# Kernel tuning notes

Measured on AMD Instinct MI355X. Metric: run time of the kernel, lower is better.

Reference implementation:

```python
import jax, jax.numpy as jnp
from jax import lax
import numpy as np

D_MODEL = 512
D_STATE = 16
D_CONV = 4
EXPAND = 2
D_INNER = EXPAND * D_MODEL  # 1024
DT_RANK = (D_MODEL + 15) // 16  # 32
FF_DIM = 1024
N_LAYERS = 2
B, L = 2, 2048


def setup_inputs() -> dict:
    key = jax.random.key(0)
    ks = jax.random.split(key, 16)
    s = 0.02
    x = jax.random.normal(ks[0], (B, L, D_MODEL), jnp.float32)
    in_proj_w = jax.random.normal(ks[1], (N_LAYERS, 2 * D_INNER, D_MODEL), jnp.float32) * s
    conv_w = jax.random.normal(ks[2], (N_LAYERS, D_INNER, D_CONV), jnp.float32) * 0.3
    conv_b = jax.random.normal(ks[3], (N_LAYERS, D_INNER), jnp.float32) * s
    x_proj_w = jax.random.normal(ks[4], (N_LAYERS, DT_RANK + 2 * D_STATE, D_INNER), jnp.float32) * s
    dt_proj_w = jax.random.normal(ks[5], (N_LAYERS, D_INNER, DT_RANK), jnp.float32) * s
    dt_proj_b = jax.random.normal(ks[6], (N_LAYERS, D_INNER), jnp.float32) * 0.5 - 4.0
    A_log = jnp.log(jnp.broadcast_to(jnp.arange(1, D_STATE + 1, dtype=jnp.float32), (N_LAYERS, D_INNER, D_STATE)))
    Dp = jnp.ones((N_LAYERS, D_INNER), jnp.float32)
    out_proj_w = jax.random.normal(ks[7], (N_LAYERS, D_MODEL, D_INNER), jnp.float32) * s
    mlp_w1 = jax.random.normal(ks[8], (FF_DIM, D_MODEL), jnp.float32) * s
    mlp_b1 = jnp.zeros((FF_DIM,), jnp.float32)
    mlp_w2 = jax.random.normal(ks[9], (D_MODEL, FF_DIM), jnp.float32) * s
    mlp_b2 = jnp.zeros((D_MODEL,), jnp.float32)
    return dict(x=x, in_proj_w=in_proj_w, conv_w=conv_w, conv_b=conv_b,
                x_proj_w=x_proj_w, dt_proj_w=dt_proj_w, dt_proj_b=dt_proj_b,
                A_log=A_log, Dp=Dp, out_proj_w=out_proj_w,
                mlp_w1=mlp_w1, mlp_b1=mlp_b1, mlp_w2=mlp_w2, mlp_b2=mlp_b2)


def _mamba_layer(x, ipw, cw, cb, xpw, dpw, dpb, Al, Dv, opw):
    # x: [B, L, d_model]
    b, l, _ = x.shape
    xz = jnp.einsum('bld,ed->ble', x, ipw)           # [B, L, 2*d_inner]
    xin, z = jnp.split(xz, 2, axis=-1)
    # causal depthwise conv1d (pad left d_conv-1)
    xc = jnp.transpose(xin, (0, 2, 1))               # [B, d_inner, L]
    xc = lax.conv_general_dilated(xc, cw[:, None, :], (1,), [(D_CONV - 1, 0)],
                                  feature_group_count=D_INNER)
    xin = jax.nn.silu(jnp.transpose(xc + cb[:, None], (0, 2, 1)))  # [B, L, d_inner]
    dbl = jnp.einsum('bld,ed->ble', xin, xpw)        # [B, L, dt_rank + 2*d_state]
    dt, Bm, Cm = jnp.split(dbl, [DT_RANK, DT_RANK + D_STATE], axis=-1)
    dt = jax.nn.softplus(jnp.einsum('blr,dr->bld', dt, dpw) + dpb)  # [B, L, d_inner]
    A = -jnp.exp(Al)                                  # [d_inner, d_state]
    dA = jnp.exp(dt[..., None] * A)                   # [B, L, d_inner, d_state]
    dBu = dt[..., None] * Bm[:, :, None, :] * xin[..., None]

    def step(h, inp):
        dA_t, dBu_t = inp
        h = dA_t * h + dBu_t
        return h, h

    h0 = jnp.zeros((b, D_INNER, D_STATE), x.dtype)
    _, hs = lax.scan(step, h0, (jnp.moveaxis(dA, 1, 0), jnp.moveaxis(dBu, 1, 0)))
    hs = jnp.moveaxis(hs, 0, 1)                       # [B, L, d_inner, d_state]
    y = jnp.einsum('blds,bls->bld', hs, Cm) + xin * Dv
    y = y * jax.nn.silu(z)
    return jnp.einsum('ble,de->bld', y, opw)


def reference(x, in_proj_w, conv_w, conv_b, x_proj_w, dt_proj_w, dt_proj_b,
              A_log, Dp, out_proj_w, mlp_w1, mlp_b1, mlp_w2, mlp_b2):
    residual = x
    for i in range(N_LAYERS):
        x = _mamba_layer(x, in_proj_w[i], conv_w[i], conv_b[i], x_proj_w[i],
                         dt_proj_w[i], dt_proj_b[i], A_log[i], Dp[i], out_proj_w[i])
    h = x + residual
    h = jax.nn.relu(jnp.einsum('bld,fd->blf', h, mlp_w1) + mlp_b1)  # dropout is identity in eval
    return jnp.einsum('blf,df->bld', h, mlp_w2) + mlp_b2
```

## Files before the change

### kernel.cpp

```cpp
#include <hip/hip_runtime.h>
#include <hip/hip_bf16.h>

#define BB 2
#define LL 2048
#define DMODEL 512
#define DSTATE 16
#define DINNER 1024
#define DTRANK 32
#define FFDIM 1024
#define MTOT (BB*LL)
#define SCL 64
#define NCC 32

typedef unsigned short u16;
typedef __attribute__((ext_vector_type(8))) short bf16x8;
typedef __attribute__((ext_vector_type(4))) float f32x4;

__device__ __forceinline__ float b2f(u16 u){
  unsigned v = ((unsigned)u) << 16; float f; __builtin_memcpy(&f, &v, 4); return f;
}
__device__ __forceinline__ u16 f2b(float f){
  unsigned u; __builtin_memcpy(&u, &f, 4);
  unsigned r = (u + 0x7FFFu + ((u >> 16) & 1u)) >> 16;
  return (u16)r;
}
__device__ __forceinline__ float siluf(float x){ return x / (1.f + __expf(-x)); }
__device__ __forceinline__ float softplusf(float v){
  return fmaxf(v, 0.f) + __logf(1.f + __expf(-fabsf(v)));
}

__device__ __forceinline__ float ldin(const void* p, size_t i, int bf){
  if (bf) return b2f(((const u16*)p)[i]);
  return ((const float*)p)[i];
}
__device__ __forceinline__ void stout(void* p, size_t i, int bf, float v){
  if (bf) ((u16*)p)[i] = f2b(v);
  else    ((float*)p)[i] = v;
}

__device__ __forceinline__ int getbf(const void* dp){
  return (*(const unsigned*)dp == 0x3F803F80u) ? 1 : 0;
}

typedef __attribute__((address_space(1))) const unsigned int gu32;
typedef __attribute__((address_space(3))) unsigned int lu32;
__device__ __forceinline__ void gl_lds16(const void* g, void* l){
  __builtin_amdgcn_global_load_lds((gu32*)g, (lu32*)l, 16, 0, 0);
}

template<int CVT>
__device__ __forceinline__ bf16x8 ld8(const void* P, size_t gi, int bf){
  if (!CVT || bf) return *(const bf16x8*)((const u16*)P + gi);
  float4 f0 = *(const float4*)((const float*)P + gi);
  float4 f1 = *(const float4*)((const float*)P + gi + 4);
  union { u16 u[8]; bf16x8 v; } t;
  t.u[0]=f2b(f0.x); t.u[1]=f2b(f0.y); t.u[2]=f2b(f0.z); t.u[3]=f2b(f0.w);
  t.u[4]=f2b(f1.x); t.u[5]=f2b(f1.y); t.u[6]=f2b(f1.z); t.u[7]=f2b(f1.w);
  return t.v;
}

#define CVT_IPW (2*2*DINNER*DMODEL)
#define CVT_XPW (2*64*DINNER)
#define CVT_DPW (2*DINNER*DTRANK)
#define CVT_OPW (2*DMODEL*DINNER)
#define CVT_W1  (FFDIM*DMODEL)
#define CVT_W2  (DMODEL*FFDIM)
#define CVT_CW  (2*DINNER*4)
#define CVT_CB  (2*DINNER)
#define CVT_TOT (CVT_IPW+CVT_XPW+CVT_DPW+CVT_OPW+CVT_W1+CVT_W2+CVT_CW+CVT_CB)
__global__ __launch_bounds__(256) void cvt_all_k(
    const void* __restrict__ ipw, const void* __restrict__ xpw,
    const void* __restrict__ dpw, const void* __restrict__ opw,
    const void* __restrict__ w1, const void* __restrict__ w2,
    const void* __restrict__ cw, const void* __restrict__ cb,
    u16* __restrict__ dst, const void* __restrict__ dprobe)
{
  const int bf = getbf(dprobe);
  size_t i4 = ((size_t)blockIdx.x * 256 + threadIdx.x) * 4;
  if (i4 >= CVT_TOT) return;
  const void* src; size_t off = i4;
  if      (off < CVT_IPW)                     { src = ipw; }
  else if ((off -= CVT_IPW) < CVT_XPW)        { src = xpw; }
  else if ((off -= CVT_XPW) < CVT_DPW)        { src = dpw; }
  else if ((off -= CVT_DPW) < CVT_OPW)        { src = opw; }
  else if ((off -= CVT_OPW) < CVT_W1)         { src = w1; }
  else if ((off -= CVT_W1)  < CVT_W2)         { src = w2; }
  else if ((off -= CVT_W2)  < CVT_CW)         { src = cw; }
  else     { off -= CVT_CW;                     src = cb; }
  ushort4 o;
  if (bf) {
    o = *(const ushort4*)((const u16*)src + off);
  } else {
    float4 f = *(const float4*)((const float*)src + off);
    o.x = f2b(f.x); o.y = f2b(f.y); o.z = f2b(f.z); o.w = f2b(f.w);
  }
  *(ushort4*)(dst + i4) = o;
}

template<int ACT, int CVA, int CVW, int CIN, int BM, int BN, int RESID, int GL>
__global__ __launch_bounds__(256) void gemm_mfma(
    const void* __restrict__ A, size_t aoff, int lda,
    const void* __restrict__ W, size_t woff,
    const void* __restrict__ bias, size_t boff,
    void* __restrict__ C, size_t coff, int ldc, int K,
    const void* __restrict__ xres, size_t xroff,
    const void* __restrict__ dprobe)
{
  const int bf = getbf(dprobe);
  constexpr int AL = BM / 64, WL = BN / 64;
  __shared__ __align__(16) u16 As[2][BM * 32];
  __shared__ __align__(16) u16 Ws[2][BN * 32];
  const int tid = threadIdx.x;
  const int row0 = blockIdx.y * BM, col0 = blockIdx.x * BN;
  const int wave = tid >> 6, lane = tid & 63;
  const int l15 = lane & 15, quad = lane >> 4;
  constexpr int WMT = (BM == 64) ? 1 : ((BN == 128) ? 4 : 2);
  const int mbase = (BM == 64) ? (wave * 16)
                  : ((BN == 128) ? (wave & 1) * 64 : wave * 32);
  const int nbase = (BM == 128 && BN == 128) ? (wave >> 1) * 64 : 0;

  const int rT = tid >> 2, csw = tid & 3;
  const int scg = csw ^ ((rT >> 1) & 3);
  const int lws = rT * 32 + csw * 8;
  const size_t ab0 = aoff + (size_t)(row0 + rT) * lda + scg * 8;
  const size_t wb0 = woff + (size_t)(col0 + rT) * K   + scg * 8;

  f32x4 acc[WMT][4];
#pragma unroll
  for (int i = 0; i < WMT; i++)
#pragma unroll
    for (int j = 0; j < 4; j++) acc[i][j] = (f32x4){0.f,0.f,0.f,0.f};

  const int NT = K >> 5;

  auto compute = [&](int cur_){
    bf16x8 af_[WMT], bf_[4];
#pragma unroll
    for (int mt = 0; mt < WMT; mt++) {
      int r_ = mbase + mt * 16 + l15;
      af_[mt] = *(const bf16x8*)&As[cur_][r_ * 32 + ((quad ^ ((r_ >> 1) & 3)) << 3)];
    }
#pragma unroll
    for (int nt = 0; nt < 4; nt++) {
      int r_ = nbase + nt * 16 + l15;
      bf_[nt] = *(const bf16x8*)&Ws[cur_][r_ * 32 + ((quad ^ ((r_ >> 1) & 3)) << 3)];
    }
#pragma unroll
    for (int mt = 0; mt < WMT; mt++)
#pragma unroll
      for (int nt = 0; nt < 4; nt++)
        acc[mt][nt] = __builtin_amdgcn_mfma_f32_16x16x32_bf16(af_[mt], bf_[nt], acc[mt][nt], 0, 0, 0);
  };

  if constexpr (GL) {
    const int wvu = __builtin_amdgcn_readfirstlane(wave);
    auto stage = [&](int buf_, int t_){
      const int kk_ = t_ * 32;
#pragma unroll
      for (int i = 0; i < AL; i++)
        gl_lds16((const u16*)A + ab0 + kk_ + (size_t)i * 64 * lda,
                 &As[buf_][i * 2048 + wvu * 512]);
#pragma unroll
      for (int i = 0; i < WL; i++)
        gl_lds16((const u16*)W + wb0 + kk_ + (size_t)i * 64 * K,
                 &Ws[buf_][i * 2048 + wvu * 512]);
    };
    stage(0, 0);
    __syncthreads();
    int cur = 0;
    for (int t = 0; t < NT; ++t) {
      if (t + 1 < NT) stage(cur ^ 1, t + 1);
      compute(cur);
      __syncthreads();
      cur ^= 1;
    }
  } else {
    bf16x8 ra0[AL], rw0[WL], ra1[AL], rw1[WL];

#define GLOAD(RA, RW, T) do { const int k1_ = (T) * 32;                        \
  _Pragma("unroll") for (int i = 0; i < AL; i++)                               \
    RA[i] = ld8<CVA>(A, ab0 + k1_ + (size_t)i * 64 * lda, bf);                 \
  _Pragma("unroll") for (int i = 0; i < WL; i++)                               \
    RW[i] = ld8<CVW>(W, wb0 + k1_ + (size_t)i * 64 * K, bf); } while (0)

#define GSTEP(RA, RW, T) do {                                                  \
  const int cur_ = (T) & 1;                                                    \
  _Pragma("unroll") for (int i = 0; i < AL; i++)                               \
    *(bf16x8*)&As[cur_][i * 2048 + lws] = RA[i];                               \
  _Pragma("unroll") for (int i = 0; i < WL; i++)                               \
    *(bf16x8*)&Ws[cur_][i * 2048 + lws] = RW[i];                               \
  if ((T) + 2 < NT) GLOAD(RA, RW, (T) + 2);                                    \
  __syncthreads();                                                             \
  compute(cur_);                                                               \
} while (0)

    GLOAD(ra0, rw0, 0);
    if (NT > 1) GLOAD(ra1, rw1, 1);
    int t = 0;
    for (; t + 1 < NT; t += 2) { GSTEP(ra0, rw0, t); GSTEP(ra1, rw1, t + 1); }
    if (t < NT) GSTEP(ra0, rw0, t);
#undef GLOAD
#undef GSTEP
  }

#pragma unroll
  for (int nt = 0; nt < 4; nt++) {
    int c = col0 + nbase + nt * 16 + l15;
    float bv = bias ? ldin(bias, boff + c, bf) : 0.f;
#pragma unroll
    for (int mt = 0; mt < WMT; mt++) {
      int rb = row0 + mbase + mt * 16 + quad * 4;
#pragma unroll
      for (int r = 0; r < 4; r++) {
        float v = acc[mt][nt][r] + bv;
        if (ACT == 1) v = softplusf(v);
        if (ACT == 2) v = fmaxf(v, 0.f);
        size_t ci = (size_t)(rb + r) * ldc + c;
        if (RESID) v += ldin(xres, xroff + ci, bf);
        if (CIN) stout(C, coff + ci, bf, v);
        else     ((u16*)C)[coff + ci] = f2b(v);
      }
    }
  }
}

template<int FST>
__global__ __launch_bounds__(256) void conv_k(
    const u16* __restrict__ xz, const void* __restrict__ cw, size_t cwo,
    const void* __restrict__ cb, size_t cbo, u16* __restrict__ xc,
    const void* __restrict__ dprobe)
{
  if (FST) {
    const u16* cw16 = (const u16*)cw;
    const u16* cb16 = (const u16*)cb;
    int idx8 = (blockIdx.x * 256 + threadIdx.x) * 8;
    int d8 = idx8 & 1023;
    int row = idx8 >> 10;
    int lb = row & (LL - 1);
    bf16x8 cwv0 = *(const bf16x8*)&cw16[cwo + d8*4];
    bf16x8 cwv1 = *(const bf16x8*)&cw16[cwo + d8*4 + 8];
    bf16x8 cwv2 = *(const bf16x8*)&cw16[cwo + d8*4 + 16];
    bf16x8 cwv3 = *(const bf16x8*)&cw16[cwo + d8*4 + 24];
    bf16x8 cbv  = *(const bf16x8*)&cb16[cbo + d8];
    bf16x8 xv0 = (bf16x8){0,0,0,0,0,0,0,0}, xv1 = xv0, xv2 = xv0, xv3 = xv0;
    if (lb >= 3) xv0 = *(const bf16x8*)&xz[(size_t)(row - 3) * 2048 + d8];
    if (lb >= 2) xv1 = *(const bf16x8*)&xz[(size_t)(row - 2) * 2048 + d8];
    if (lb >= 1) xv2 = *(const bf16x8*)&xz[(size_t)(row - 1) * 2048 + d8];
    xv3 = *(const bf16x8*)&xz[(size_t)row * 2048 + d8];
    bf16x8 ov;
#pragma unroll
    for (int i = 0; i < 8; i++) {
      float acc = b2f((u16)cbv[i]);
      int c0 = i * 4;
      float w0 = b2f((u16)((c0 < 8) ? cwv0[c0 & 7] : (c0 < 16) ? cwv1[c0 & 7] : (c0 < 24) ? cwv2[c0 & 7] : cwv3[c0 & 7]));
      float w1_ = b2f((u16)(((c0+1) < 8) ? cwv0[(c0+1) & 7] : ((c0+1) < 16) ? cwv1[(c0+1) & 7] : ((c0+1) < 24) ? cwv2[(c0+1) & 7] : cwv3[(c0+1) & 7]));
      float w2_ = b2f((u16)(((c0+2) < 8) ? cwv0[(c0+2) & 7] : ((c0+2) < 16) ? cwv1[(c0+2) & 7] : ((c0+2) < 24) ? cwv2[(c0+2) & 7] : cwv3[(c0+2) & 7]));
      float w3_ = b2f((u16)(((c0+3) < 8) ? cwv0[(c0+3) & 7] : ((c0+3) < 16) ? cwv1[(c0+3) & 7] : ((c0+3) < 24) ? cwv2[(c0+3) & 7] : cwv3[(c0+3) & 7]));
      acc += w0 * b2f((u16)xv0[i]);
      acc += w1_ * b2f((u16)xv1[i]);
      acc += w2_ * b2f((u16)xv2[i]);
      acc += w3_ * b2f((u16)xv3[i]);
      ov[i] = (short)f2b(siluf(acc));
    }
    *(bf16x8*)&xc[idx8] = ov;
  } else {
    const int bf = getbf(dprobe);
    int idx = blockIdx.x * 256 + threadIdx.x;
    int d = idx & 1023;
    int row = idx >> 10;
    int lb = row & (LL - 1);
    float acc = ldin(cb, cbo + d, bf);
#pragma unroll
    for (int k = 0; k < 4; k++) {
      int lk = lb - 3 + k;
      if (lk >= 0) acc += ldin(cw, cwo + d*4 + k, bf) * b2f(xz[(size_t)(row - 3 + k) * 2048 + d]);
    }
    xc[idx] = f2b(siluf(acc));
  }
}

template<int CVW>
__global__ __launch_bounds__(256) void scan_A_k(
    const u16* __restrict__ xc,
    const u16* __restrict__ dbl,
    const void* __restrict__ dpwp, size_t dpwo,
    const void* __restrict__ dpbp, size_t dpbo,
    const void* __restrict__ Alog, size_t alo,
    float* __restrict__ Pc, float* __restrict__ Sc,
    const void* __restrict__ dprobe)
{
  const int bf = getbf(dprobe);
  int bid = blockIdx.x;
  int b = bid >> 9;
  int c = (bid >> 4) & (NCC - 1);
  int g = bid & 15;
  int t = threadIdx.x;
  int dl = t >> 2, sq = t & 3;
  int d0 = g * 64, d = d0 + dl;
  int rowb = b * LL + c * SCL;

  __shared__ __align__(16) u16 dts[64 * 64];
  __shared__ __align__(16) u16 us[64 * 64];
  __shared__ __align__(16) float Bs[64 * 20];
  u16* dbls = dts;
  u16* dpws = dts + 64 * 32;

  {
    int r = t >> 2, c8 = (t & 3) * 8;
    *(bf16x8*)&dbls[r * 32 + c8] =
        *(const bf16x8*)&dbl[(size_t)(rowb + r) * 64 + c8];
    *(bf16x8*)&dpws[r * 32 + c8] =
        ld8<CVW>(dpwp, dpwo + (size_t)(d0 + r) * DTRANK + c8, bf);
  }
#pragma unroll
  for (int p = 0; p < 2; p++) {
    int seg = p * 256 + t;
    int r = seg >> 3, c8 = (seg & 7) * 8;
    bf16x8 uv = *(const bf16x8*)&xc[(size_t)(rowb + r) * 1024 + d0 + c8];
    int coff = r >> 3, roff = r & 7;
#pragma unroll
    for (int i = 0; i < 8; i++) {
      int dd = c8 + i;
      us[dd * 64 + ((coff ^ (dd & 7)) << 3) + roff] = (u16)uv[i];
    }
  }
  if (t < 128) {
    int l = t >> 1, grp = t & 1;
    bf16x8 v = *(const bf16x8*)&dbl[(size_t)(rowb + l) * 64 + 32 + grp * 8];
    f32x4 f0 = {b2f((u16)v[0]), b2f((u16)v[1]), b2f((u16)v[2]), b2f((u16)v[3])};
    f32x4 f1 = {b2f((u16)v[4]), b2f((u16)v[5]), b2f((u16)v[6]), b2f((u16)v[7])};
    *(f32x4*)&Bs[l * 20 + grp * 8]     = f0;
    *(f32x4*)&Bs[l * 20 + grp * 8 + 4] = f1;
  }
  float Av[4];
#pragma unroll
  for (int j = 0; j < 4; j++)
    Av[j] = -__expf(ldin(Alog, alo + (size_t)d * DSTATE + sq * 4 + j, bf));
  __syncthreads();

  {
    int wv = t >> 6, lane = t & 63;
    int fl = lane & 15, qd = lane >> 4;
    bf16x8 afr  = *(const bf16x8*)&dbls[(wv * 16 + fl) * 32 + qd * 8];
    bf16x8 bfr0 = *(const bf16x8*)&dpws[(fl)      * 32 + qd * 8];
    bf16x8 bfr1 = *(const bf16x8*)&dpws[(16 + fl) * 32 + qd * 8];
    bf16x8 bfr2 = *(const bf16x8*)&dpws[(32 + fl) * 32 + qd * 8];
    bf16x8 bfr3 = *(const bf16x8*)&dpws[(48 + fl) * 32 + qd * 8];
    __syncthreads();
    f32x4 zz = {0.f, 0.f, 0.f, 0.f};
    f32x4 a0 = __builtin_amdgcn_mfma_f32_16x16x32_bf16(afr, bfr0, zz, 0, 0, 0);
    f32x4 a1 = __builtin_amdgcn_mfma_f32_16x16x32_bf16(afr, bfr1, zz, 0, 0, 0);
    f32x4 a2 = __builtin_amdgcn_mfma_f32_16x16x32_bf16(afr, bfr2, zz, 0, 0, 0);
    f32x4 a3 = __builtin_amdgcn_mfma_f32_16x16x32_bf16(afr, bfr3, zz, 0, 0, 0);
    int lc = wv * 2 + (qd >> 1);
    int off = (qd & 1) * 4;
#define DTWR(AN, NT) do {                                                      \
    int dd_ = (NT) * 16 + fl;                                                  \
    float bvv_ = ldin(dpbp, dpbo + d0 + dd_, bf);                              \
    ushort4 pk_;                                                               \
    pk_.x = f2b(softplusf(AN[0] + bvv_));                                      \
    pk_.y = f2b(softplusf(AN[1] + bvv_));                                      \
    pk_.z = f2b(softplusf(AN[2] + bvv_));                                      \
    pk_.w = f2b(softplusf(AN[3] + bvv_));                                      \
    *(ushort4*)&dts[dd_ * 64 + ((lc ^ (dd_ & 7)) << 3) + off] = pk_; } while (0)
    DTWR(a0, 0); DTWR(a1, 1); DTWR(a2, 2); DTWR(a3, 3);
#undef DTWR
  }
  __syncthreads();

  float h[4] = {0.f,0.f,0.f,0.f}, P[4] = {1.f,1.f,1.f,1.f};
  for (int cc = 0; cc < 8; cc++) {
    int base = dl * 64 + ((cc ^ (dl & 7)) << 3);
    bf16x8 dt8 = *(const bf16x8*)&dts[base];
    bf16x8 u8  = *(const bf16x8*)&us[base];
#pragma unroll
    for (int i = 0; i < 8; i++) {
      int l = cc * 8 + i;
      float dtv = b2f((u16)dt8[i]);
      float uv  = b2f((u16)u8[i]);
      float dtu = dtv * uv;
      f32x4 B4 = *(const f32x4*)&Bs[l * 20 + sq * 4];
#pragma unroll
      for (int j = 0; j < 4; j++) {
        float dA = __expf(dtv * Av[j]);
        h[j] = dA * h[j] + dtu * B4[j];
        P[j] *= dA;
      }
    }
  }
  size_t o = (((size_t)b * DINNER + d) * NCC + c) * DSTATE + sq * 4;
  *(f32x4*)&Pc[o] = (f32x4){P[0], P[1], P[2], P[3]};
  *(f32x4*)&Sc[o] = (f32x4){h[0], h[1], h[2], h[3]};
}

__global__ __launch_bounds__(256) void scan_B_k(
    float* __restrict__ Pc, const float* __restrict__ Sc)
{
  int idx = blockIdx.x * 256 + threadIdx.x;
  int bd = idx >> 4, s = idx & 15;
  float h = 0.f;
  for (int c = 0; c < NCC; c++) {
    size_t o = ((size_t)bd * NCC + c) * DSTATE + s;
    float P = Pc[o], S = Sc[o];
    Pc[o] = h;
    h = P * h + S;
  }
}

template<int CVW>
__global__ __launch_bounds__(256) void scan_C_k(
    u16* __restrict__ dtp, int sdt, const u16* __restrict__ xz,
    const u16* __restrict__ xc,
    const u16* __restrict__ dbl,
    const void* __restrict__ dpwp, size_t dpwo,
    const void* __restrict__ dpbp, size_t dpbo,
    const void* __restrict__ Alog, size_t alo,
    const void* __restrict__ Dpt, size_t dpo, const float* __restrict__ Hinit,
    const void* __restrict__ dprobe)
{
  const int bf = getbf(dprobe);
  int bid = blockIdx.x;
  int b = bid >> 9;
  int c = (bid >> 4) & (NCC - 1);
  int g = bid & 15;
  int t = threadIdx.x;
  int dl = t >> 2, sq = t & 3;
  int d0 = g * 64, d = d0 + dl;
  int rowb = b * LL + c * SCL;

  __shared__ __align__(16) u16 dts[64 * 64];
  __shared__ __align__(16) u16 us[64 * 64];
  __shared__ __align__(16) u16 outs[64 * 64];
  __shared__ __align__(16) float BCs[64 * 36];
  u16* dbls = dts;
  u16* dpws = dts + 64 * 32;

  {
    int r = t >> 2, c8 = (t & 3) * 8;
    *(bf16x8*)&dbls[r * 32 + c8] =
        *(const bf16x8*)&dbl[(size_t)(rowb + r) * 64 + c8];
    *(bf16x8*)&dpws[r * 32 + c8] =
        ld8<CVW>(dpwp, dpwo + (size_t)(d0 + r) * DTRANK + c8, bf);
  }
#pragma unroll
  for (int p = 0; p < 2; p++) {
    int seg = p * 256 + t;
    int r = seg >> 3, c8 = (seg & 7) * 8;
    bf16x8 uv = *(const bf16x8*)&xc[(size_t)(rowb + r) * 1024 + d0 + c8];
    int coff = r >> 3, roff = r & 7;
#pragma unroll
    for (int i = 0; i < 8; i++) {
      int dd = c8 + i;
      us[dd * 64 + ((coff ^ (dd & 7)) << 3) + roff] = (u16)uv[i];
    }
  }
  {
    int l = t >> 2, grp = t & 3;
    bf16x8 v = *(const bf16x8*)&dbl[(size_t)(rowb + l) * 64 + 32 + grp * 8];
    f32x4 f0 = {b2f((u16)v[0]), b2f((u16)v[1]), b2f((u16)v[2]), b2f((u16)v[3])};
    f32x4 f1 = {b2f((u16)v[4]), b2f((u16)v[5]), b2f((u16)v[6]), b2f((u16)v[7])};
    *(f32x4*)&BCs[l * 36 + grp * 8]     = f0;
    *(f32x4*)&BCs[l * 36 + grp * 8 + 4] = f1;
  }
  float Av[4];
#pragma unroll
  for (int j = 0; j < 4; j++)
    Av[j] = -__expf(ldin(Alog, alo + (size_t)d * DSTATE + sq * 4 + j, bf));
  float Dv = ldin(Dpt, dpo + d, bf);
  float h[4];
  size_t o = (((size_t)b * DINNER + d) * NCC + c) * DSTATE + sq * 4;
  f32x4 h4 = *(const f32x4*)&Hinit[o];
  h[0] = h4[0]; h[1] = h4[1]; h[2] = h4[2]; h[3] = h4[3];
  __syncthreads();

  {
    int wv = t >> 6, lane = t & 63;
    int fl = lane & 15, qd = lane >> 4;
    bf16x8 afr  = *(const bf16x8*)&dbls[(wv * 16 + fl) * 32 + qd * 8];
    bf16x8 bfr0 = *(const bf16x8*)&dpws[(fl)      * 32 + qd * 8];
    bf16x8 bfr1 = *(const bf16x8*)&dpws[(16 + fl) * 32 + qd * 8];
    bf16x8 bfr2 = *(const bf16x8*)&dpws[(32 + fl) * 32 + qd * 8];
    bf16x8 bfr3 = *(const bf16x8*)&dpws[(48 + fl) * 32 + qd * 8];
    __syncthreads();
    f32x4 zz = {0.f, 0.f, 0.f, 0.f};
    f32x4 a0 = __builtin_amdgcn_mfma_f32_16x16x32_bf16(afr, bfr0, zz, 0, 0, 0);
    f32x4 a1 = __builtin_amdgcn_mfma_f32_16x16x32_bf16(afr, bfr1, zz, 0, 0, 0);
    f32x4 a2 = __builtin_amdgcn_mfma_f32_16x16x32_bf16(afr, bfr2, zz, 0, 0, 0);
    f32x4 a3 = __builtin_amdgcn_mfma_f32_16x16x32_bf16(afr, bfr3, zz, 0, 0, 0);
    int lc = wv * 2 + (qd >> 1);
    int off = (qd & 1) * 4;
#define DTWR(AN, NT) do {                                                      \
    int dd_ = (NT) * 16 + fl;                                                  \
    float bvv_ = ldin(dpbp, dpbo + d0 + dd_, bf);                              \
    ushort4 pk_;                                                               \
    pk_.x = f2b(softplusf(AN[0] + bvv_));                                      \
    pk_.y = f2b(softplusf(AN[1] + bvv_));                                      \
    pk_.z = f2b(softplusf(AN[2] + bvv_));                                      \
    pk_.w = f2b(softplusf(AN[3] + bvv_));                                      \
    *(ushort4*)&dts[dd_ * 64 + ((lc ^ (dd_ & 7)) << 3) + off] = pk_; } while (0)
    DTWR(a0, 0); DTWR(a1, 1); DTWR(a2, 2); DTWR(a3, 3);
#undef DTWR
  }
  __syncthreads();

  for (int cc = 0; cc < 8; cc++) {
    int base = dl * 64 + ((cc ^ (dl & 7)) << 3);
    bf16x8 dt8 = *(const bf16x8*)&dts[base];
    bf16x8 u8  = *(const bf16x8*)&us[base];
#pragma unroll
    for (int i = 0; i < 8; i++) {
      int l = cc * 8 + i;
      float dtv = b2f((u16)dt8[i]);
      float uv  = b2f((u16)u8[i]);
      float dtu = dtv * uv;
      f32x4 B4 = *(const f32x4*)&BCs[l * 36 + sq * 4];
      f32x4 C4 = *(const f32x4*)&BCs[l * 36 + 16 + sq * 4];
      float y = 0.f;
#pragma unroll
      for (int j = 0; j < 4; j++) {
        float dA = __expf(dtv * Av[j]);
        h[j] = dA * h[j] + dtu * B4[j];
        y += h[j] * C4[j];
      }
      y += __shfl_xor(y, 1);
      y += __shfl_xor(y, 2);
      if (sq == 0) outs[l * 64 + dl] = f2b(y + uv * Dv);
    }
  }
  __syncthreads();
#pragma unroll
  for (int p = 0; p < 2; p++) {
    int seg = p * 256 + t;
    int r = seg >> 3, c8 = (seg & 7) * 8;
    bf16x8 yv = *(const bf16x8*)&outs[r * 64 + c8];
    bf16x8 zv = *(const bf16x8*)&xz[(size_t)(rowb + r) * 2048 + 1024 + d0 + c8];
    bf16x8 ov;
#pragma unroll
    for (int i = 0; i < 8; i++) {
      float z = b2f((u16)zv[i]);
      ov[i] = (short)f2b(b2f((u16)yv[i]) * siluf(z));
    }
    *(bf16x8*)&dtp[(size_t)(rowb + r) * sdt + d0 + c8] = ov;
  }
}

extern "C" void kernel_launch(void* const* d_in, const int* in_sizes, int n_in,
                              void* d_out, int out_size, void* d_ws, size_t ws_size,
                              hipStream_t stream) {
  const void* x_in = d_in[0];
  const void* ipw  = d_in[1];
  const void* cw   = d_in[2];
  const void* cb   = d_in[3];
  const void* xpw  = d_in[4];
  const void* dpw  = d_in[5];
  const void* dpb  = d_in[6];
  const void* Alog = d_in[7];
  const void* Dpt  = d_in[8];
  const void* opw  = d_in[9];
  const void* w1   = d_in[10];
  const void* b1   = d_in[11];
  const void* w2   = d_in[12];
  const void* b2   = d_in[13];

  const bool full = ws_size >= (size_t)64 * 1024 * 1024;

  if (full) {
    float* Pc = (float*)((char*)d_ws + 64);
    float* Sc = Pc + (size_t)BB*DINNER*NCC*DSTATE;
    u16* p = (u16*)(Sc + (size_t)BB*DINNER*NCC*DSTATE);
    u16* cvt0  = p;
    u16* ipw16 = p;  p += (size_t)CVT_IPW;
    u16* xpw16 = p;  p += (size_t)CVT_XPW;
    u16* dpw16 = p;  p += (size_t)CVT_DPW;
    u16* opw16 = p;  p += (size_t)CVT_OPW;
    u16* w116  = p;  p += (size_t)CVT_W1;
    u16* w216  = p;  p += (size_t)CVT_W2;
    u16* cw16  = p;  p += (size_t)CVT_CW;
    u16* cb16  = p;  p += (size_t)CVT_CB;
    u16* xz    = p;  p += (size_t)MTOT*2*DINNER;
    u16* xc    = p;  p += (size_t)MTOT*DINNER;
    u16* dty   = p;  p += (size_t)MTOT*DINNER;
    u16* dbl   = p;
    u16* bx = xc;
    u16* resid = xz;
    u16* hid = xz + (size_t)4*1024*1024;

    cvt_all_k<<<(CVT_TOT/4 + 255)/256, 256, 0, stream>>>(
        ipw, xpw, dpw, opw, w1, w2, cw, cb, cvt0, Dpt);

    for (int layer = 0; layer < 2; layer++) {
      size_t ipw_o = (size_t)layer*2*DINNER*DMODEL;
      size_t cw_o  = (size_t)layer*DINNER*4,  cb_o = (size_t)layer*DINNER;
      size_t xpw_o = (size_t)layer*64*DINNER, dpw_o = (size_t)layer*DINNER*DTRANK;
      size_t dpb_o = (size_t)layer*DINNER,    al_o = (size_t)layer*DINNER*DSTATE;
      size_t dp_o  = (size_t)layer*DINNER,    opw_o = (size_t)layer*DMODEL*DINNER;
      if (layer == 0)
        gemm_mfma<0,1,0,0,128,128,0,0><<<dim3(16, 32), 256, 0, stream>>>(
            x_in, 0, DMODEL, ipw16, ipw_o, nullptr, 0, xz, 0, 2048, DMODEL,
            nullptr, 0, Dpt);
      else
        gemm_mfma<0,0,0,0,128,128,0,1><<<dim3(16, 32), 256, 0, stream>>>(
            bx, 0, DMODEL, ipw16, ipw_o, nullptr, 0, xz, 0, 2048, DMODEL,
            nullptr, 0, Dpt);
      conv_k<1><<<MTOT*DINNER/2048, 256, 0, stream>>>(
          xz, cw16, cw_o, cb16, cb_o, xc, Dpt);
      gemm_mfma<0,0,0,0,64,64,0,1><<<dim3(1, 64), 256, 0, stream>>>(
          xc, 0, DINNER, xpw16, xpw_o, nullptr, 0, dbl, 0, 64, DINNER,
          nullptr, 0, Dpt);
      scan_A_k<0><<<BB*NCC*16, 256, 0, stream>>>(
          xc, dbl, dpw16, dpw_o, dpb, dpb_o, Alog, al_o, Pc, Sc, Dpt);
      scan_B_k<<<BB*64, 256, 0, stream>>>(Pc, Sc);
      scan_C_k<0><<<BB*NCC*16, 256, 0, stream>>>(
          dty, 1024, xz, xc, dbl, dpw16, dpw_o, dpb, dpb_o, Alog, al_o,
          Dpt, dp_o, Pc, Dpt);
      if (layer == 0)
        gemm_mfma<0,0,0,0,64,64,0,1><<<dim3(8, 64), 256, 0, stream>>>(
            dty, 0, 1024, opw16, opw_o, nullptr, 0, bx, 0, DMODEL, DINNER,
            nullptr, 0, Dpt);
      else
        gemm_mfma<0,0,0,0,64,64,1,1><<<dim3(8, 64), 256, 0, stream>>>(
            dty, 0, 1024, opw16, opw_o, nullptr, 0, resid, 0, DMODEL, DINNER,
            x_in, 0, Dpt);
    }
    gemm_mfma<2,0,0,0,64,64,0,1><<<dim3(16, 64), 256, 0, stream>>>(
        resid, 0, DMODEL, w116, 0, b1, 0, hid, 0, FFDIM, DMODEL,
        nullptr, 0, Dpt);
    gemm_mfma<0,0,0,1,64,64,0,1><<<dim3(8, 64), 256, 0, stream>>>(
        hid, 0, FFDIM, w216, 0, b2, 0, d_out, 0, DMODEL, FFDIM,
        nullptr, 0, Dpt);
  } else {
    float* Pc = (float*)((char*)d_ws + 64);
    float* Sc = Pc + (size_t)DINNER*NCC*DSTATE;
    u16* p = (u16*)(Sc + (size_t)DINNER*NCC*DSTATE);
    u16* xz  = p;  p += (size_t)LL*2*DINNER;
    u16* xc  = p;  p += (size_t)LL*DINNER;
    u16* bxF = p;  p += (size_t)MTOT*DMODEL;
    u16* dbl = p;
    u16* hid = xz + (size_t)2*1024*1024;

    for (int layer = 0; layer < 2; layer++) {
      size_t ipw_o = (size_t)layer*2*DINNER*DMODEL;
      size_t cw_o  = (size_t)layer*DINNER*4,  cb_o = (size_t)layer*DINNER;
      size_t xpw_o = (size_t)layer*64*DINNER, dpw_o = (size_t)layer*DINNER*DTRANK;
      size_t dpb_o = (size_t)layer*DINNER,    al_o = (size_t)layer*DINNER*DSTATE;
      size_t dp_o  = (size_t)layer*DINNER,    opw_o = (size_t)layer*DMODEL*DINNER;
      for (int b = 0; b < BB; b++) {
        size_t ro = (size_t)b * LL * DMODEL;
        if (layer == 0)
          gemm_mfma<0,1,1,0,128,128,0,0><<<dim3(16, 16), 256, 0, stream>>>(
              x_in, ro, DMODEL, ipw, ipw_o, nullptr, 0, xz, 0, 2048, DMODEL,
              nullptr, 0, Dpt);
        else
          gemm_mfma<0,0,1,0,128,128,0,0><<<dim3(16, 16), 256, 0, stream>>>(
              bxF, ro, DMODEL, ipw, ipw_o, nullptr, 0, xz, 0, 2048, DMODEL,
              nullptr, 0, Dpt);
        conv_k<0><<<LL*DINNER/256, 256, 0, stream>>>(xz, cw, cw_o, cb, cb_o, xc, Dpt);
        gemm_mfma<0,0,1,0,64,64,0,0><<<dim3(1, 32), 256, 0, stream>>>(
            xc, 0, DINNER, xpw, xpw_o, nullptr, 0, dbl, 0, 64, DINNER,
            nullptr, 0, Dpt);
        scan_A_k<1><<<NCC*16, 256, 0, stream>>>(
            xc, dbl, dpw, dpw_o, dpb, dpb_o, Alog, al_o, Pc, Sc, Dpt);
        scan_B_k<<<64, 256, 0, stream>>>(Pc, Sc);
        scan_C_k<1><<<NCC*16, 256, 0, stream>>>(
            xz, 2048, xz, xc, dbl, dpw, dpw_o, dpb, dpb_o, Alog, al_o,
            Dpt, dp_o, Pc, Dpt);
        if (layer == 0)
          gemm_mfma<0,0,1,0,64,64,0,0><<<dim3(8, 32), 256, 0, stream>>>(
              xz, 0, 2048, opw, opw_o, nullptr, 0, bxF, ro, DMODEL, DINNER,
              nullptr, 0, Dpt);
        else
          gemm_mfma<0,0,1,0,64,64,1,0><<<dim3(8, 32), 256, 0, stream>>>(
              xz, 0, 2048, opw, opw_o, nullptr, 0, bxF, ro, DMODEL, DINNER,
              x_in, ro, Dpt);
      }
    }
    for (int b = 0; b < BB; b++) {
      size_t ro = (size_t)b * LL * DMODEL;
      gemm_mfma<2,0,1,0,64,64,0,0><<<dim3(16, 32), 256, 0, stream>>>(
          bxF, ro, DMODEL, w1, 0, b1, 0, hid, 0, FFDIM, DMODEL,
          nullptr, 0, Dpt);
      gemm_mfma<0,0,1,1,64,64,0,0><<<dim3(8, 32), 256, 0, stream>>>(
          hid, 0, FFDIM, w2, 0, b2, 0, d_out, ro, DMODEL, FFDIM,
          nullptr, 0, Dpt);
    }
  }
}
```

Baseline: 348.9 us.

## Use K=64 GEMM tiles, fold chunk-carry scan into scan_C, skip weight conversion for bf16

Removes the global_load_lds path from the GEMM and adds a KB template parameter so the 64x64 GEMMs stage 64-wide K tiles with an XOR swizzle over 8 chunks, halving the number of barrier-separated K steps. The scan_B kernel is dropped and each scan_C block now recomputes its own incoming state by serially combining the chunk prefix values of all earlier chunks. When the inputs are already bf16, the weight-conversion kernel is skipped and the raw weight pointers are used directly. The trade-offs are more LDS per block, redundant prefix work in later chunks, and a register-loaded path replacing async LDS loads.

```diff
diff --git a/kernel.cpp b/kernel.cpp
--- a/kernel.cpp
+++ b/kernel.cpp
@@ -40,12 +40,6 @@
 
 __device__ __forceinline__ int getbf(const void* dp){
   return (*(const unsigned*)dp == 0x3F803F80u) ? 1 : 0;
-}
-
-typedef __attribute__((address_space(1))) const unsigned int gu32;
-typedef __attribute__((address_space(3))) unsigned int lu32;
-__device__ __forceinline__ void gl_lds16(const void* g, void* l){
-  __builtin_amdgcn_global_load_lds((gu32*)g, (lu32*)l, 16, 0, 0);
 }
 
 template<int CVT>
@@ -97,7 +91,7 @@
   *(ushort4*)(dst + i4) = o;
 }
 
-template<int ACT, int CVA, int CVW, int CIN, int BM, int BN, int RESID, int GL>
+template<int ACT, int CVA, int CVW, int CIN, int BM, int BN, int KB, int RESID>
 __global__ __launch_bounds__(256) void gemm_mfma(
     const void* __restrict__ A, size_t aoff, int lda,
     const void* __restrict__ W, size_t woff,
@@ -107,9 +101,12 @@
     const void* __restrict__ dprobe)
 {
   const int bf = getbf(dprobe);
-  constexpr int AL = BM / 64, WL = BN / 64;
-  __shared__ __align__(16) u16 As[2][BM * 32];
-  __shared__ __align__(16) u16 Ws[2][BN * 32];
+  constexpr int C8  = KB / 8;
+  constexpr int TR  = 256 / C8;
+  constexpr int ALD = BM / TR;
+  constexpr int WLD = BN / TR;
+  __shared__ __align__(16) u16 As[2][BM * KB];
+  __shared__ __align__(16) u16 Ws[2][BN * KB];
   const int tid = threadIdx.x;
   const int row0 = blockIdx.y * BM, col0 = blockIdx.x * BN;
   const int wave = tid >> 6, lane = tid & 63;
@@ -119,9 +116,9 @@
                   : ((BN == 128) ? (wave & 1) * 64 : wave * 32);
   const int nbase = (BM == 128 && BN == 128) ? (wave >> 1) * 64 : 0;
 
-  const int rT = tid >> 2, csw = tid & 3;
-  const int scg = csw ^ ((rT >> 1) & 3);
-  const int lws = rT * 32 + csw * 8;
+  const int rT = tid / C8, csw = tid % C8;
+  const int scg = (KB == 32) ? (csw ^ ((rT >> 1) & 3)) : (csw ^ (rT & 7));
+  const int lws = tid * 8;
   const size_t ab0 = aoff + (size_t)(row0 + rT) * lda + scg * 8;
   const size_t wb0 = woff + (size_t)(col0 + rT) * K   + scg * 8;
 
@@ -131,77 +128,59 @@
 #pragma unroll
     for (int j = 0; j < 4; j++) acc[i][j] = (f32x4){0.f,0.f,0.f,0.f};
 
-  const int NT = K >> 5;
-
+  const int NT = K / KB;
+
+  auto fchunk = [&](int r_, int g){
+    return (KB == 32) ? (g ^ ((r_ >> 1) & 3)) : (g ^ (r_ & 7));
+  };
   auto compute = [&](int cur_){
-    bf16x8 af_[WMT], bf_[4];
-#pragma unroll
-    for (int mt = 0; mt < WMT; mt++) {
-      int r_ = mbase + mt * 16 + l15;
-      af_[mt] = *(const bf16x8*)&As[cur_][r_ * 32 + ((quad ^ ((r_ >> 1) & 3)) << 3)];
-    }
-#pragma unroll
-    for (int nt = 0; nt < 4; nt++) {
-      int r_ = nbase + nt * 16 + l15;
-      bf_[nt] = *(const bf16x8*)&Ws[cur_][r_ * 32 + ((quad ^ ((r_ >> 1) & 3)) << 3)];
-    }
-#pragma unroll
-    for (int mt = 0; mt < WMT; mt++)
-#pragma unroll
-      for (int nt = 0; nt < 4; nt++)
-        acc[mt][nt] = __builtin_amdgcn_mfma_f32_16x16x32_bf16(af_[mt], bf_[nt], acc[mt][nt], 0, 0, 0);
+#pragma unroll
+    for (int ks = 0; ks < KB / 32; ks++) {
+      bf16x8 af_[WMT], bf_[4];
+#pragma unroll
+      for (int mt = 0; mt < WMT; mt++) {
+        int r_ = mbase + mt * 16 + l15;
+        af_[mt] = *(const bf16x8*)&As[cur_][r_ * KB + fchunk(r_, ks * 4 + quad) * 8];
+      }
+#pragma unroll
+      for (int nt = 0; nt < 4; nt++) {
+        int r_ = nbase + nt * 16 + l15;
+        bf_[nt] = *(const bf16x8*)&Ws[cur_][r_ * KB + fchunk(r_, ks * 4 + quad) * 8];
+      }
+#pragma unroll
+      for (int mt = 0; mt < WMT; mt++)
+#pragma unroll
+        for (int nt = 0; nt < 4; nt++)
+          acc[mt][nt] = __builtin_amdgcn_mfma_f32_16x16x32_bf16(af_[mt], bf_[nt], acc[mt][nt], 0, 0, 0);
+    }
   };
 
-  if constexpr (GL) {
-    const int wvu = __builtin_amdgcn_readfirstlane(wave);
-    auto stage = [&](int buf_, int t_){
-      const int kk_ = t_ * 32;
-#pragma unroll
-      for (int i = 0; i < AL; i++)
-        gl_lds16((const u16*)A + ab0 + kk_ + (size_t)i * 64 * lda,
-                 &As[buf_][i * 2048 + wvu * 512]);
-#pragma unroll
-      for (int i = 0; i < WL; i++)
-        gl_lds16((const u16*)W + wb0 + kk_ + (size_t)i * 64 * K,
-                 &Ws[buf_][i * 2048 + wvu * 512]);
-    };
-    stage(0, 0);
-    __syncthreads();
-    int cur = 0;
-    for (int t = 0; t < NT; ++t) {
-      if (t + 1 < NT) stage(cur ^ 1, t + 1);
-      compute(cur);
-      __syncthreads();
-      cur ^= 1;
-    }
-  } else {
-    bf16x8 ra0[AL], rw0[WL], ra1[AL], rw1[WL];
-
-#define GLOAD(RA, RW, T) do { const int k1_ = (T) * 32;                        \
-  _Pragma("unroll") for (int i = 0; i < AL; i++)                               \
-    RA[i] = ld8<CVA>(A, ab0 + k1_ + (size_t)i * 64 * lda, bf);                 \
-  _Pragma("unroll") for (int i = 0; i < WL; i++)                               \
-    RW[i] = ld8<CVW>(W, wb0 + k1_ + (size_t)i * 64 * K, bf); } while (0)
+  bf16x8 ra0[ALD], rw0[WLD], ra1[ALD], rw1[WLD];
+
+#define GLOAD(RA, RW, T) do { const int k1_ = (T) * KB;                        \
+  _Pragma("unroll") for (int i = 0; i < ALD; i++)                              \
+    RA[i] = ld8<CVA>(A, ab0 + k1_ + (size_t)i * TR * lda, bf);                 \
+  _Pragma("unroll") for (int i = 0; i < WLD; i++)                              \
+    RW[i] = ld8<CVW>(W, wb0 + k1_ + (size_t)i * TR * K, bf); } while (0)
 
 #define GSTEP(RA, RW, T) do {                                                  \
   const int cur_ = (T) & 1;                                                    \
-  _Pragma("unroll") for (int i = 0; i < AL; i++)                               \
-    *(bf16x8*)&As[cur_][i * 2048 + lws] = RA[i];                               \
-  _Pragma("unroll") for (int i = 0; i < WL; i++)                               \
-    *(bf16x8*)&Ws[cur_][i * 2048 + lws] = RW[i];                               \
+  _Pragma("unroll") for (int i = 0; i < ALD; i++)                              \
+    *(bf16x8*)&As[cur_][lws + i * 2048] = RA[i];                               \
+  _Pragma("unroll") for (int i = 0; i < WLD; i++)                              \
+    *(bf16x8*)&Ws[cur_][lws + i * 2048] = RW[i];                               \
   if ((T) + 2 < NT) GLOAD(RA, RW, (T) + 2);                                    \
   __syncthreads();                                                             \
   compute(cur_);                                                               \
 } while (0)
 
-    GLOAD(ra0, rw0, 0);
-    if (NT > 1) GLOAD(ra1, rw1, 1);
-    int t = 0;
-    for (; t + 1 < NT; t += 2) { GSTEP(ra0, rw0, t); GSTEP(ra1, rw1, t + 1); }
-    if (t < NT) GSTEP(ra0, rw0, t);
+  GLOAD(ra0, rw0, 0);
+  if (NT > 1) GLOAD(ra1, rw1, 1);
+  int t = 0;
+  for (; t + 1 < NT; t += 2) { GSTEP(ra0, rw0, t); GSTEP(ra1, rw1, t + 1); }
+  if (t < NT) GSTEP(ra0, rw0, t);
 #undef GLOAD
 #undef GSTEP
-  }
 
 #pragma unroll
   for (int nt = 0; nt < 4; nt++) {
@@ -393,20 +372,6 @@
   *(f32x4*)&Sc[o] = (f32x4){h[0], h[1], h[2], h[3]};
 }
 
-__global__ __launch_bounds__(256) void scan_B_k(
-    float* __restrict__ Pc, const float* __restrict__ Sc)
-{
-  int idx = blockIdx.x * 256 + threadIdx.x;
-  int bd = idx >> 4, s = idx & 15;
-  float h = 0.f;
-  for (int c = 0; c < NCC; c++) {
-    size_t o = ((size_t)bd * NCC + c) * DSTATE + s;
-    float P = Pc[o], S = Sc[o];
-    Pc[o] = h;
-    h = P * h + S;
-  }
-}
-
 template<int CVW>
 __global__ __launch_bounds__(256) void scan_C_k(
     u16* __restrict__ dtp, int sdt, const u16* __restrict__ xz,
@@ -415,7 +380,8 @@
     const void* __restrict__ dpwp, size_t dpwo,
     const void* __restrict__ dpbp, size_t dpbo,
     const void* __restrict__ Alog, size_t alo,
-    const void* __restrict__ Dpt, size_t dpo, const float* __restrict__ Hinit,
+    const void* __restrict__ Dpt, size_t dpo,
+    const float* __restrict__ Pcp, const float* __restrict__ Scp,
     const void* __restrict__ dprobe)
 {
   const int bf = getbf(dprobe);
@@ -467,10 +433,16 @@
   for (int j = 0; j < 4; j++)
     Av[j] = -__expf(ldin(Alog, alo + (size_t)d * DSTATE + sq * 4 + j, bf));
   float Dv = ldin(Dpt, dpo + d, bf);
-  float h[4];
-  size_t o = (((size_t)b * DINNER + d) * NCC + c) * DSTATE + sq * 4;
-  f32x4 h4 = *(const f32x4*)&Hinit[o];
-  h[0] = h4[0]; h[1] = h4[1]; h[2] = h4[2]; h[3] = h4[3];
+  float h[4] = {0.f, 0.f, 0.f, 0.f};
+  {
+    size_t ob = (((size_t)b * DINNER + d) * NCC) * DSTATE + sq * 4;
+    for (int c2 = 0; c2 < c; c2++) {
+      f32x4 P4 = *(const f32x4*)&Pcp[ob + (size_t)c2 * DSTATE];
+      f32x4 S4 = *(const f32x4*)&Scp[ob + (size_t)c2 * DSTATE];
+#pragma unroll
+      for (int j = 0; j < 4; j++) h[j] = P4[j] * h[j] + S4[j];
+    }
+  }
   __syncthreads();
 
   {
@@ -563,6 +535,7 @@
   const void* b2   = d_in[13];
 
   const bool full = ws_size >= (size_t)64 * 1024 * 1024;
+  const bool bfh = (in_sizes[1] == (int)(CVT_IPW * 2));
 
   if (full) {
     float* Pc = (float*)((char*)d_ws + 64);
@@ -585,8 +558,17 @@
     u16* resid = xz;
     u16* hid = xz + (size_t)4*1024*1024;
 
-    cvt_all_k<<<(CVT_TOT/4 + 255)/256, 256, 0, stream>>>(
-        ipw, xpw, dpw, opw, w1, w2, cw, cb, cvt0, Dpt);
+    const u16* Wipw = bfh ? (const u16*)ipw : ipw16;
+    const u16* Wxpw = bfh ? (const u16*)xpw : xpw16;
+    const u16* Wdpw = bfh ? (const u16*)dpw : dpw16;
+    const u16* Wopw = bfh ? (const u16*)opw : opw16;
+    const u16* Ww1  = bfh ? (const u16*)w1  : w116;
+    const u16* Ww2  = bfh ? (const u16*)w2  : w216;
+    const u16* Wcw  = bfh ? (const u16*)cw  : cw16;
+    const u16* Wcb  = bfh ? (const u16*)cb  : cb16;
+    if (!bfh)
+      cvt_all_k<<<(CVT_TOT/4 + 255)/256, 256, 0, stream>>>(
+          ipw, xpw, dpw, opw, w1, w2, cw, cb, cvt0, Dpt);
 
     for (int layer = 0; layer < 2; layer++) {
       size_t ipw_o = (size_t)layer*2*DINNER*DMODEL;
@@ -595,38 +577,37 @@
       size_t dpb_o = (size_t)layer*DINNER,    al_o = (size_t)layer*DINNER*DSTATE;
       size_t dp_o  = (size_t)layer*DINNER,    opw_o = (size_t)layer*DMODEL*DINNER;
       if (layer == 0)
-        gemm_mfma<0,1,0,0,128,128,0,0><<<dim3(16, 32), 256, 0, stream>>>(
-            x_in, 0, DMODEL, ipw16, ipw_o, nullptr, 0, xz, 0, 2048, DMODEL,
+        gemm_mfma<0,1,0,0,128,128,32,0><<<dim3(16, 32), 256, 0, stream>>>(
+            x_in, 0, DMODEL, Wipw, ipw_o, nullptr, 0, xz, 0, 2048, DMODEL,
             nullptr, 0, Dpt);
       else
-        gemm_mfma<0,0,0,0,128,128,0,1><<<dim3(16, 32), 256, 0, stream>>>(
-            bx, 0, DMODEL, ipw16, ipw_o, nullptr, 0, xz, 0, 2048, DMODEL,
+        gemm_mfma<0,0,0,0,128,128,32,0><<<dim3(16, 32), 256, 0, stream>>>(
+            bx, 0, DMODEL, Wipw, ipw_o, nullptr, 0, xz, 0, 2048, DMODEL,
             nullptr, 0, Dpt);
       conv_k<1><<<MTOT*DINNER/2048, 256, 0, stream>>>(
-          xz, cw16, cw_o, cb16, cb_o, xc, Dpt);
-      gemm_mfma<0,0,0,0,64,64,0,1><<<dim3(1, 64), 256, 0, stream>>>(
-          xc, 0, DINNER, xpw16, xpw_o, nullptr, 0, dbl, 0, 64, DINNER,
+          xz, Wcw, cw_o, Wcb, cb_o, xc, Dpt);
+      gemm_mfma<0,0,0,0,64,64,64,0><<<dim3(1, 64), 256, 0, stream>>>(
+          xc, 0, DINNER, Wxpw, xpw_o, nullptr, 0, dbl, 0, 64, DINNER,
           nullptr, 0, Dpt);
       scan_A_k<0><<<BB*NCC*16, 256, 0, stream>>>(
-          xc, dbl, dpw16, dpw_o, dpb, dpb_o, Alog, al_o, Pc, Sc, Dpt);
-      scan_B_k<<<BB*64, 256, 0, stream>>>(Pc, Sc);
+          xc, dbl, Wdpw, dpw_o, dpb, dpb_o, Alog, al_o, Pc, Sc, Dpt);
       scan_C_k<0><<<BB*NCC*16, 256, 0, stream>>>(
-          dty, 1024, xz, xc, dbl, dpw16, dpw_o, dpb, dpb_o, Alog, al_o,
-          Dpt, dp_o, Pc, Dpt);
+          dty, 1024, xz, xc, dbl, Wdpw, dpw_o, dpb, dpb_o, Alog, al_o,
+          Dpt, dp_o, Pc, Sc, Dpt);
       if (layer == 0)
-        gemm_mfma<0,0,0,0,64,64,0,1><<<dim3(8, 64), 256, 0, stream>>>(
-            dty, 0, 1024, opw16, opw_o, nullptr, 0, bx, 0, DMODEL, DINNER,
+        gemm_mfma<0,0,0,0,64,64,64,0><<<dim3(8, 64), 256, 0, stream>>>(
+            dty, 0, 1024, Wopw, opw_o, nullptr, 0, bx, 0, DMODEL, DINNER,
             nullptr, 0, Dpt);
       else
-        gemm_mfma<0,0,0,0,64,64,1,1><<<dim3(8, 64), 256, 0, stream>>>(
-            dty, 0, 1024, opw16, opw_o, nullptr, 0, resid, 0, DMODEL, DINNER,
+        gemm_mfma<0,0,0,0,64,64,64,1><<<dim3(8, 64), 256, 0, stream>>>(
+            dty, 0, 1024, Wopw, opw_o, nullptr, 0, resid, 0, DMODEL, DINNER,
             x_in, 0, Dpt);
     }
-    gemm_mfma<2,0,0,0,64,64,0,1><<<dim3(16, 64), 256, 0, stream>>>(
-        resid, 0, DMODEL, w116, 0, b1, 0, hid, 0, FFDIM, DMODEL,
+    gemm_mfma<2,0,0,0,64,64,64,0><<<dim3(16, 64), 256, 0, stream>>>(
+        resid, 0, DMODEL, Ww1, 0, b1, 0, hid, 0, FFDIM, DMODEL,
         nullptr, 0, Dpt);
-    gemm_mfma<0,0,0,1,64,64,0,1><<<dim3(8, 64), 256, 0, stream>>>(
-        hid, 0, FFDIM, w216, 0, b2, 0, d_out, 0, DMODEL, FFDIM,
+    gemm_mfma<0,0,0,1,64,64,64,0><<<dim3(8, 64), 256, 0, stream>>>(
+        hid, 0, FFDIM, Ww2, 0, b2, 0, d_out, 0, DMODEL, FFDIM,
         nullptr, 0, Dpt);
   } else {
     float* Pc = (float*)((char*)d_ws + 64);
@@ -647,39 +628,38 @@
       for (int b = 0; b < BB; b++) {
         size_t ro = (size_t)b * LL * DMODEL;
         if (layer == 0)
-          gemm_mfma<0,1,1,0,128,128,0,0><<<dim3(16, 16), 256, 0, stream>>>(
+          gemm_mfma<0,1,1,0,128,128,32,0><<<dim3(16, 16), 256, 0, stream>>>(
               x_in, ro, DMODEL, ipw, ipw_o, nullptr, 0, xz, 0, 2048, DMODEL,
               nullptr, 0, Dpt);
         else
-          gemm_mfma<0,0,1,0,128,128,0,0><<<dim3(16, 16), 256, 0, stream>>>(
+          gemm_mfma<0,0,1,0,128,128,32,0><<<dim3(16, 16), 256, 0, stream>>>(
               bxF, ro, DMODEL, ipw, ipw_o, nullptr, 0, xz, 0, 2048, DMODEL,
               nullptr, 0, Dpt);
         conv_k<0><<<LL*DINNER/256, 256, 0, stream>>>(xz, cw, cw_o, cb, cb_o, xc, Dpt);
-        gemm_mfma<0,0,1,0,64,64,0,0><<<dim3(1, 32), 256, 0, stream>>>(
+        gemm_mfma<0,0,1,0,64,64,64,0><<<dim3(1, 32), 256, 0, stream>>>(
             xc, 0, DINNER, xpw, xpw_o, nullptr, 0, dbl, 0, 64, DINNER,
             nullptr, 0, Dpt);
         scan_A_k<1><<<NCC*16, 256, 0, stream>>>(
             xc, dbl, dpw, dpw_o, dpb, dpb_o, Alog, al_o, Pc, Sc, Dpt);
-        scan_B_k<<<64, 256, 0, stream>>>(Pc, Sc);
         scan_C_k<1><<<NCC*16, 256, 0, stream>>>(
             xz, 2048, xz, xc, dbl, dpw, dpw_o, dpb, dpb_o, Alog, al_o,
-            Dpt, dp_o, Pc, Dpt);
+            Dpt, dp_o, Pc, Sc, Dpt);
         if (layer == 0)
-          gemm_mfma<0,0,1,0,64,64,0,0><<<dim3(8, 32), 256, 0, stream>>>(
+          gemm_mfma<0,0,1,0,64,64,64,0><<<dim3(8, 32), 256, 0, stream>>>(
               xz, 0, 2048, opw, opw_o, nullptr, 0, bxF, ro, DMODEL, DINNER,
               nullptr, 0, Dpt);
         else
-          gemm_mfma<0,0,1,0,64,64,1,0><<<dim3(8, 32), 256, 0, stream>>>(
+          gemm_mfma<0,0,1,0,64,64,64,1><<<dim3(8, 32), 256, 0, stream>>>(
               xz, 0, 2048, opw, opw_o, nullptr, 0, bxF, ro, DMODEL, DINNER,
               x_in, ro, Dpt);
       }
     }
     for (int b = 0; b < BB; b++) {
       size_t ro = (size_t)b * LL * DMODEL;
-      gemm_mfma<2,0,1,0,64,64,0,0><<<dim3(16, 32), 256, 0, stream>>>(
+      gemm_mfma<2,0,1,0,64,64,64,0><<<dim3(16, 32), 256, 0, stream>>>(
           bxF, ro, DMODEL, w1, 0, b1, 0, hid, 0, FFDIM, DMODEL,
           nullptr, 0, Dpt);
-      gemm_mfma<0,0,1,1,64,64,0,0><<<dim3(8, 32), 256, 0, stream>>>(
+      gemm_mfma<0,0,1,1,64,64,64,0><<<dim3(8, 32), 256, 0, stream>>>(
           hid, 0, FFDIM, w2, 0, b2, 0, d_out, ro, DMODEL, FFDIM,
           nullptr, 0, Dpt);
     }
```

After: 340.1 us. -2.5%, faster.
